# Performance work log

Measured on AMD Instinct MI355X. Metric: run time of the kernel, lower is better.

## Reference

```python
import jax, jax.numpy as jnp
import numpy as np

B, S, HID = 4, 8192, 1024
H, D = 16, 64
CHUNK = 64
N_BEFORE, N_AFTER = 1, 0
MASK_VALUE = -1e9


def look_adjacent(x, n_before, n_after):
    # x: [B, H, n_chunks, chunk, ...] -> concat rolled neighbor chunks along chunk-len dim
    if n_before == 0 and n_after == 0:
        return x
    slices = [jnp.roll(x, shift=-i, axis=2) for i in range(-n_before, n_after + 1)]
    return jnp.concatenate(slices, axis=3)


def setup_inputs() -> dict:
    key = jax.random.key(0)
    k0, k1, k2, k3 = jax.random.split(key, 4)
    scale = 1.0 / np.sqrt(HID)
    return {
        "hidden_states": jax.random.normal(k0, (B, S, HID), dtype=jnp.float32),
        "Wq": jax.random.normal(k1, (HID, HID), dtype=jnp.float32) * scale,
        "Wk": jax.random.normal(k2, (HID, HID), dtype=jnp.float32) * scale,
        "Wv": jax.random.normal(k3, (HID, HID), dtype=jnp.float32) * scale,
    }


def reference(hidden_states, Wq, Wk, Wv):
    b, s, _ = hidden_states.shape
    nC = s // CHUNK

    def split_heads(x):  # [B,S,HID] -> [B,H,S,D]
        return x.reshape(b, s, H, D).transpose(0, 2, 1, 3)

    q = split_heads(hidden_states @ Wq)
    k = split_heads(hidden_states @ Wk) / jnp.sqrt(jnp.asarray(D, hidden_states.dtype))
    v = split_heads(hidden_states @ Wv)

    # chunk: [B,H,nC,C,D]
    q = q.reshape(b, H, nC, CHUNK, D)
    k = k.reshape(b, H, nC, CHUNK, D)
    v = v.reshape(b, H, nC, CHUNK, D)

    idx = jnp.broadcast_to(jnp.arange(s), (b, H, s)).reshape(b, H, nC, CHUNK)
    q_idx = idx
    k_idx = look_adjacent(idx, N_BEFORE, N_AFTER)  # [B,H,nC,(1+nb+na)*C]
    k = look_adjacent(k, N_BEFORE, N_AFTER)        # [B,H,nC,(1+nb+na)*C,D]
    v = look_adjacent(v, N_BEFORE, N_AFTER)

    dots = jnp.einsum("bhncd,bhnkd->bhnck", q, k)  # [B,H,nC,C,K]
    causal = q_idx[..., :, None] >= k_idx[..., None, :]  # is_decoder causal mask
    dots = jnp.where(causal, dots, jnp.asarray(MASK_VALUE, dots.dtype))

    probs = jax.nn.softmax(dots, axis=-1)
    out = jnp.einsum("bhnck,bhnkd->bhncd", probs, v)  # [B,H,nC,C,D]
    out = out.reshape(b, H, s, D).transpose(0, 2, 1, 3).reshape(b, s, H * D)
    return out
```

## Files before the change

kernel.cpp:

```cpp
#include <hip/hip_runtime.h>
#include <hip/hip_bf16.h>

#define NB 4
#define NS 8192
#define NHID 1024
#define NH 16
#define ND 64
#define NCHUNK 128

typedef __attribute__((ext_vector_type(8))) __bf16 bf16x8;
typedef __attribute__((ext_vector_type(4))) float f32x4;

__device__ __forceinline__ unsigned short f2bf(float x) {
  unsigned int u = __builtin_bit_cast(unsigned int, x);
  unsigned int r = (u + 0x7FFFu + ((u >> 16) & 1u)) >> 16;
  return (unsigned short)r;
}

__device__ __forceinline__ void gload16(const void* g, void* l) {
  __builtin_amdgcn_global_load_lds(
      (const __attribute__((address_space(1))) unsigned int*)g,
      (__attribute__((address_space(3))) unsigned int*)l, 16, 0, 0);
}

#define BAR()                        \
  asm volatile("" ::: "memory");     \
  __builtin_amdgcn_s_barrier();      \
  asm volatile("" ::: "memory")

__global__ __launch_bounds__(256) void convert_x(const float* __restrict__ x,
                                                 unsigned short* __restrict__ xb) {
  int gt = blockIdx.x * 256 + threadIdx.x;
  const float4* xf = (const float4*)x;
  float4 v0 = xf[gt * 2 + 0];
  float4 v1 = xf[gt * 2 + 1];
  uint4 o;
  o.x = f2bf(v0.x) | ((unsigned)f2bf(v0.y) << 16);
  o.y = f2bf(v0.z) | ((unsigned)f2bf(v0.w) << 16);
  o.z = f2bf(v1.x) | ((unsigned)f2bf(v1.y) << 16);
  o.w = f2bf(v1.z) | ((unsigned)f2bf(v1.w) << 16);
  ((uint4*)xb)[gt] = o;
}

__global__ __launch_bounds__(256) void transpose_w(const float* __restrict__ w0,
                                                   const float* __restrict__ w1,
                                                   const float* __restrict__ w2,
                                                   unsigned short* __restrict__ wt) {
  __shared__ float tile[32][33];
  int wi = blockIdx.z;
  const float* w = (wi == 0) ? w0 : ((wi == 1) ? w1 : w2);
  float scale = (wi == 1) ? 0.125f : 1.0f;
  int k0 = blockIdx.x * 32, n0 = blockIdx.y * 32;
  int tx = threadIdx.x, ty = threadIdx.y;
#pragma unroll
  for (int i = 0; i < 4; i++)
    tile[ty + i * 8][tx] = w[(k0 + ty + i * 8) * NHID + n0 + tx];
  __syncthreads();
#pragma unroll
  for (int i = 0; i < 4; i++)
    wt[(wi * NHID + n0 + ty + i * 8) * NHID + k0 + tx] =
        f2bf(tile[tx][ty + i * 8] * scale);
}

#define OFF_A0 0
#define OFF_A1 16384
#define OFF_B0 32768
#define OFF_B1 49152

__device__ __forceinline__ void stage_half(const unsigned short* __restrict__ src,
                                           size_t row0, int kt, char* ldsbase,
                                           int tid) {
#pragma unroll
  for (int i = 0; i < 2; i++) {
    int g = tid + i * 512;
    int r = g >> 3;
    int slot = (g & 7) ^ (r & 7);
    gload16(src + (row0 + r) * NHID + kt * 64 + slot * 8, ldsbase + g * 16);
  }
}

__device__ __forceinline__ bf16x8 lds_frag(const char* base, int r, int ks,
                                           int lg) {
  int byte = (r * 128 + ks * 64 + lg * 16) ^ ((r & 7) << 4);
  return *reinterpret_cast<const bf16x8*>(base + byte);
}

#define MFMA16(ACC, AF, BF)                                                  \
  __builtin_amdgcn_s_setprio(1);                                            \
  _Pragma("unroll") for (int mi = 0; mi < 4; mi++)                          \
      _Pragma("unroll") for (int ni = 0; ni < 2; ni++)                      \
          _Pragma("unroll") for (int ks = 0; ks < 2; ks++)                  \
              ACC[mi][ni] = __builtin_amdgcn_mfma_f32_16x16x32_bf16(        \
                  AF[mi][ks], BF[ni][ks], ACC[mi][ni], 0, 0, 0);            \
  __builtin_amdgcn_s_setprio(0)

__global__ __launch_bounds__(512, 2) void gemm_qkv(
    const unsigned short* __restrict__ xb, const unsigned short* __restrict__ wt,
    unsigned short* __restrict__ qg, unsigned short* __restrict__ kg,
    unsigned short* __restrict__ vg) {
  __shared__ alignas(16) char smem[131072];
  int bid = blockIdx.x;
  int wg = (bid & 7) * 192 + (bid >> 3);
  int bm = wg / 12, bn = wg % 12;
  int tid = threadIdx.x;
  int l = tid & 63, lg = l >> 4, lm = l & 15;
  int w = tid >> 6, wm = w >> 2, wn = w & 3;

  const size_t arow0 = (size_t)bm * 256;
  const size_t brow0 = (size_t)bn * 256;

  stage_half(xb, arow0, 0, smem + OFF_A0, tid);
  stage_half(wt, brow0, 0, smem + OFF_B0, tid);
  stage_half(xb, arow0 + 128, 0, smem + OFF_A1, tid);
  stage_half(wt, brow0 + 128, 0, smem + OFF_B1, tid);
  stage_half(xb, arow0, 1, smem + 65536 + OFF_A0, tid);
  stage_half(wt, brow0, 1, smem + 65536 + OFF_B0, tid);
  asm volatile("s_waitcnt vmcnt(4)" ::: "memory");
  BAR();

  f32x4 acc[2][2][4][2] = {};
  bf16x8 a[4][2], b0[2][2], b1[2][2];

#pragma unroll 1
  for (int t = 0; t < 16; ++t) {
    char* cb = smem + (t & 1) * 65536;
    char* nb = smem + ((t & 1) ^ 1) * 65536;

#pragma unroll
    for (int mi = 0; mi < 4; mi++)
#pragma unroll
      for (int ks = 0; ks < 2; ks++)
        a[mi][ks] = lds_frag(cb + OFF_A0, wm * 64 + mi * 16 + lm, ks, lg);
#pragma unroll
    for (int ni = 0; ni < 2; ni++)
#pragma unroll
      for (int ks = 0; ks < 2; ks++)
        b0[ni][ks] = lds_frag(cb + OFF_B0, wn * 32 + ni * 16 + lm, ks, lg);
    if (t < 15) stage_half(xb, arow0 + 128, t + 1, nb + OFF_A1, tid);
    BAR();
    MFMA16(acc[0][0], a, b0);
    BAR();

#pragma unroll
    for (int ni = 0; ni < 2; ni++)
#pragma unroll
      for (int ks = 0; ks < 2; ks++)
        b1[ni][ks] = lds_frag(cb + OFF_B1, wn * 32 + ni * 16 + lm, ks, lg);
    if (t < 15) stage_half(wt, brow0 + 128, t + 1, nb + OFF_B1, tid);
    BAR();
    MFMA16(acc[0][1], a, b1);
    BAR();

#pragma unroll
    for (int mi = 0; mi < 4; mi++)
#pragma unroll
      for (int ks = 0; ks < 2; ks++)
        a[mi][ks] = lds_frag(cb + OFF_A1, wm * 64 + mi * 16 + lm, ks, lg);
    if (t < 14) stage_half(xb, arow0, t + 2, cb + OFF_A0, tid);
    BAR();
    MFMA16(acc[1][0], a, b0);
    BAR();

    if (t < 14) {
      stage_half(wt, brow0, t + 2, cb + OFF_B0, tid);
      asm volatile("s_waitcnt vmcnt(4)" ::: "memory");
    } else {
      asm volatile("s_waitcnt vmcnt(0)" ::: "memory");
    }
    BAR();
    MFMA16(acc[1][1], a, b1);
    BAR();
  }

  int wsel = bn >> 2;
  unsigned short* dst = (wsel == 0) ? qg : ((wsel == 1) ? kg : vg);
#pragma unroll
  for (int qm = 0; qm < 2; qm++)
#pragma unroll
    for (int qn = 0; qn < 2; qn++)
#pragma unroll
      for (int mi = 0; mi < 4; mi++)
#pragma unroll
        for (int ni = 0; ni < 2; ni++)
#pragma unroll
          for (int rr = 0; rr < 4; rr++) {
            int gm = bm * 256 + qm * 128 + wm * 64 + mi * 16 + lg * 4 + rr;
            int n = (bn & 3) * 256 + qn * 128 + wn * 32 + ni * 16 + lm;
            int b = gm >> 13, s = gm & (NS - 1);
            int h = n >> 6, d = n & (ND - 1);
            dst[(((size_t)(b * NH + h) * NS) + s) * ND + d] =
                f2bf(acc[qm][qn][mi][ni][rr]);
          }
}

__global__ __launch_bounds__(256, 4) void attn_local(
    const unsigned short* __restrict__ qg, const unsigned short* __restrict__ kg,
    const unsigned short* __restrict__ vg, float* __restrict__ out) {
  __shared__ alignas(16) char lds[40960];
  unsigned short* qs = (unsigned short*)lds;
  unsigned short* ks2 = (unsigned short*)(lds + 8192);
  unsigned short* vts = (unsigned short*)(lds + 24576);
  char* psb = lds;
  int c = blockIdx.x, h = blockIdx.y, b = blockIdx.z;
  int t = threadIdx.x;
  int w = t >> 6, l = t & 63, lg = l >> 4, lm = l & 15;
  size_t bhbase = (size_t)(b * NH + h) * NS * ND;
  int kv0 = (c - 1) * 64;

  int g0 = t, g1 = t + 256;
  int qrow0 = g0 >> 3, qcc0 = g0 & 7, qrow1 = g1 >> 3, qcc1 = g1 & 7;
  uint4 qv0 = *reinterpret_cast<const uint4*>(
      qg + bhbase + (size_t)(c * 64 + qrow0) * ND + qcc0 * 8);
  uint4 qv1 = *reinterpret_cast<const uint4*>(
      qg + bhbase + (size_t)(c * 64 + qrow1) * ND + qcc1 * 8);
  uint4 kvr[4];
  int krow[4], kcc[4];
#pragma unroll
  for (int i = 0; i < 4; i++) {
    int g = t + i * 256;
    krow[i] = g >> 3;
    kcc[i] = g & 7;
    int s = kv0 + krow[i];
    if (s < 0) s = 0;
    kvr[i] =
        *reinterpret_cast<const uint4*>(kg + bhbase + (size_t)s * ND + kcc[i] * 8);
  }
  int kq = t >> 1, half = t & 1;
  int sv = kv0 + kq;
  if (sv < 0) sv = 0;
  uint4 vreg[4];
#pragma unroll
  for (int i = 0; i < 4; i++)
    vreg[i] = *reinterpret_cast<const uint4*>(vg + bhbase + (size_t)sv * ND +
                                              half * 32 + i * 8);

  *reinterpret_cast<uint4*>(lds + ((qrow0 * 128 + qcc0 * 16) ^ ((qrow0 & 7) << 4))) =
      qv0;
  *reinterpret_cast<uint4*>(lds + ((qrow1 * 128 + qcc1 * 16) ^ ((qrow1 & 7) << 4))) =
      qv1;
#pragma unroll
  for (int i = 0; i < 4; i++)
    *reinterpret_cast<uint4*>(
        lds + 8192 + ((krow[i] * 128 + kcc[i] * 16) ^ ((krow[i] & 7) << 4))) =
        kvr[i];
  __syncthreads();

  bf16x8 qa[2];
#pragma unroll
  for (int ks = 0; ks < 2; ks++) {
    int row = w * 16 + lm;
    int byte = (row * 128 + (ks * 32 + lg * 8) * 2) ^ ((row & 7) << 4);
    qa[ks] = *reinterpret_cast<const bf16x8*>((char*)qs + byte);
  }
  f32x4 sf[8];
#pragma unroll
  for (int nt = 0; nt < 8; nt++) {
    f32x4 a = {};
#pragma unroll
    for (int ks = 0; ks < 2; ks++) {
      int n = nt * 16 + lm;
      int byte = (n * 128 + (ks * 32 + lg * 8) * 2) ^ ((n & 7) << 4);
      bf16x8 kb = *reinterpret_cast<const bf16x8*>((char*)ks2 + byte);
      a = __builtin_amdgcn_mfma_f32_16x16x32_bf16(kb, qa[ks], a, 0, 0, 0);
    }
    sf[nt] = a;
  }

  int q = w * 16 + lm;
  float m = -1e30f;
#pragma unroll
  for (int nt = 0; nt < 8; nt++)
#pragma unroll
    for (int r = 0; r < 4; r++) {
      int j = nt * 16 + lg * 4 + r;
      bool valid = (j <= q + 64) && (c > 0 || j >= 64);
      if (valid) m = fmaxf(m, sf[nt][r]);
    }
  m = fmaxf(m, __shfl_xor(m, 16, 64));
  m = fmaxf(m, __shfl_xor(m, 32, 64));

  float sum = 0.f;
#pragma unroll
  for (int nt = 0; nt < 8; nt++)
#pragma unroll
    for (int r = 0; r < 4; r++) {
      int j = nt * 16 + lg * 4 + r;
      bool valid = (j <= q + 64) && (c > 0 || j >= 64);
      float p = valid ? __expf(sf[nt][r] - m) : 0.0f;
      sf[nt][r] = p;
      sum += p;
    }
  sum += __shfl_xor(sum, 16, 64);
  sum += __shfl_xor(sum, 32, 64);
  float rn = 1.0f / sum;

  __syncthreads();

#pragma unroll
  for (int nt = 0; nt < 8; nt++) {
    unsigned int lo =
        f2bf(sf[nt][0] * rn) | ((unsigned)f2bf(sf[nt][1] * rn) << 16);
    unsigned int hi =
        f2bf(sf[nt][2] * rn) | ((unsigned)f2bf(sf[nt][3] * rn) << 16);
    int kvb = nt * 16 + lg * 4;
    int byte = (q * 256 + kvb * 2) ^ ((q & 7) << 4);
    *reinterpret_cast<uint2*>(psb + byte) = make_uint2(lo, hi);
  }
  {
    unsigned short* vtse = (unsigned short*)vts;
#pragma unroll
    for (int i = 0; i < 4; i++) {
      int d0 = half * 32 + i * 8;
      unsigned int u[4] = {vreg[i].x, vreg[i].y, vreg[i].z, vreg[i].w};
#pragma unroll
      for (int j = 0; j < 8; j++) {
        unsigned short val = (unsigned short)(u[j >> 1] >> ((j & 1) * 16));
        vtse[(d0 + j) * 128 + (kq ^ (j << 3))] = val;
      }
    }
  }
  __syncthreads();

  bf16x8 pa[4];
#pragma unroll
  for (int ks = 0; ks < 4; ks++) {
    int byte = (q * 256 + (ks * 32 + lg * 8) * 2) ^ ((q & 7) << 4);
    pa[ks] = *reinterpret_cast<const bf16x8*>(psb + byte);
  }
#pragma unroll
  for (int nt = 0; nt < 4; nt++) {
    f32x4 o = {};
#pragma unroll
    for (int ks = 0; ks < 4; ks++) {
      int dn = nt * 16 + lm;
      int byte = (dn * 256 + (ks * 32 + lg * 8) * 2) ^ ((dn & 7) << 4);
      bf16x8 vb = *reinterpret_cast<const bf16x8*>((char*)vts + byte);
      o = __builtin_amdgcn_mfma_f32_16x16x32_bf16(pa[ks], vb, o, 0, 0, 0);
    }
#pragma unroll
    for (int r = 0; r < 4; r++) {
      int sq = c * 64 + w * 16 + lg * 4 + r;
      int d = nt * 16 + lm;
      out[(size_t)(b * NS + sq) * (NH * ND) + h * ND + d] = o[r];
    }
  }
}

extern "C" void kernel_launch(void* const* d_in, const int* in_sizes, int n_in,
                              void* d_out, int out_size, void* d_ws, size_t ws_size,
                              hipStream_t stream) {
  const float* hs = (const float*)d_in[0];
  const float* wq = (const float*)d_in[1];
  const float* wk = (const float*)d_in[2];
  const float* wv = (const float*)d_in[3];
  float* out = (float*)d_out;
  char* ws = (char*)d_ws;

  const size_t XB_BYTES = (size_t)NB * NS * NHID * 2;
  const size_t WT_BYTES = (size_t)3 * NHID * NHID * 2;
  const size_t QKV_BYTES = (size_t)NB * NH * NS * ND * 2;
  unsigned short* xb = (unsigned short*)ws;
  unsigned short* wt = (unsigned short*)(ws + XB_BYTES);
  unsigned short* qg = (unsigned short*)(ws + XB_BYTES + WT_BYTES);
  unsigned short* kg = (unsigned short*)(ws + XB_BYTES + WT_BYTES + QKV_BYTES);
  unsigned short* vg = (unsigned short*)(ws + XB_BYTES + WT_BYTES + 2 * QKV_BYTES);

  hipLaunchKernelGGL(convert_x, dim3((NB * NS * NHID) / (256 * 8)), dim3(256), 0,
                     stream, hs, xb);
  hipLaunchKernelGGL(transpose_w, dim3(32, 32, 3), dim3(32, 8), 0, stream, wq, wk,
                     wv, wt);
  hipLaunchKernelGGL(gemm_qkv, dim3(128 * 12), dim3(512), 0, stream, xb, wt, qg,
                     kg, vg);
  hipLaunchKernelGGL(attn_local, dim3(NCHUNK, NH, NB), dim3(256), 0, stream, qg,
                     kg, vg, out);
}
```

Measured before the change: 498.5 us.

## Merge GEMM sub-phases to halve barriers and stage epilogue through LDS

The QKV projection GEMM main loop now issues both next-stage global-to-LDS loads up front and pairs the MFMA blocks, cutting the per-iteration barrier count from eight to four. The epilogue writes bf16 results into swizzled shared memory, then each thread stores 16-byte vectors to global instead of scattered 2-byte stores. This targets barrier stalls and uncoalesced output writes, at the cost of more live B fragments (register pressure) and an extra LDS round trip.

Result: no change. 505.3 us (+1.4%).

```diff
diff --git a/kernel.cpp b/kernel.cpp
--- a/kernel.cpp
+++ b/kernel.cpp
@@ -126,6 +126,10 @@
     char* cb = smem + (t & 1) * 65536;
     char* nb = smem + ((t & 1) ^ 1) * 65536;
 
+    if (t < 15) {
+      stage_half(xb, arow0 + 128, t + 1, nb + OFF_A1, tid);
+      stage_half(wt, brow0 + 128, t + 1, nb + OFF_B1, tid);
+    }
 #pragma unroll
     for (int mi = 0; mi < 4; mi++)
 #pragma unroll
@@ -134,63 +138,67 @@
 #pragma unroll
     for (int ni = 0; ni < 2; ni++)
 #pragma unroll
-      for (int ks = 0; ks < 2; ks++)
+      for (int ks = 0; ks < 2; ks++) {
         b0[ni][ks] = lds_frag(cb + OFF_B0, wn * 32 + ni * 16 + lm, ks, lg);
-    if (t < 15) stage_half(xb, arow0 + 128, t + 1, nb + OFF_A1, tid);
+        b1[ni][ks] = lds_frag(cb + OFF_B1, wn * 32 + ni * 16 + lm, ks, lg);
+      }
     BAR();
     MFMA16(acc[0][0], a, b0);
-    BAR();
-
-#pragma unroll
-    for (int ni = 0; ni < 2; ni++)
-#pragma unroll
-      for (int ks = 0; ks < 2; ks++)
-        b1[ni][ks] = lds_frag(cb + OFF_B1, wn * 32 + ni * 16 + lm, ks, lg);
-    if (t < 15) stage_half(wt, brow0 + 128, t + 1, nb + OFF_B1, tid);
-    BAR();
     MFMA16(acc[0][1], a, b1);
     BAR();
 
+    if (t < 14) {
+      stage_half(xb, arow0, t + 2, cb + OFF_A0, tid);
+      stage_half(wt, brow0, t + 2, cb + OFF_B0, tid);
+    }
 #pragma unroll
     for (int mi = 0; mi < 4; mi++)
 #pragma unroll
       for (int ks = 0; ks < 2; ks++)
         a[mi][ks] = lds_frag(cb + OFF_A1, wm * 64 + mi * 16 + lm, ks, lg);
-    if (t < 14) stage_half(xb, arow0, t + 2, cb + OFF_A0, tid);
-    BAR();
-    MFMA16(acc[1][0], a, b0);
-    BAR();
-
     if (t < 14) {
-      stage_half(wt, brow0, t + 2, cb + OFF_B0, tid);
       asm volatile("s_waitcnt vmcnt(4)" ::: "memory");
     } else {
       asm volatile("s_waitcnt vmcnt(0)" ::: "memory");
     }
     BAR();
+    MFMA16(acc[1][0], a, b0);
     MFMA16(acc[1][1], a, b1);
     BAR();
   }
 
+#pragma unroll
+  for (int qm = 0; qm < 2; qm++)
+#pragma unroll
+    for (int qn = 0; qn < 2; qn++)
+#pragma unroll
+      for (int mi = 0; mi < 4; mi++)
+#pragma unroll
+        for (int ni = 0; ni < 2; ni++)
+#pragma unroll
+          for (int rr = 0; rr < 4; rr++) {
+            int row = qm * 128 + wm * 64 + mi * 16 + lg * 4 + rr;
+            int col = qn * 128 + wn * 32 + ni * 16 + lm;
+            int byte = (row * 512 + col * 2) ^ ((row & 7) << 4);
+            *reinterpret_cast<unsigned short*>(smem + byte) =
+                f2bf(acc[qm][qn][mi][ni][rr]);
+          }
+  BAR();
   int wsel = bn >> 2;
   unsigned short* dst = (wsel == 0) ? qg : ((wsel == 1) ? kg : vg);
 #pragma unroll
-  for (int qm = 0; qm < 2; qm++)
-#pragma unroll
-    for (int qn = 0; qn < 2; qn++)
-#pragma unroll
-      for (int mi = 0; mi < 4; mi++)
-#pragma unroll
-        for (int ni = 0; ni < 2; ni++)
-#pragma unroll
-          for (int rr = 0; rr < 4; rr++) {
-            int gm = bm * 256 + qm * 128 + wm * 64 + mi * 16 + lg * 4 + rr;
-            int n = (bn & 3) * 256 + qn * 128 + wn * 32 + ni * 16 + lm;
-            int b = gm >> 13, s = gm & (NS - 1);
-            int h = n >> 6, d = n & (ND - 1);
-            dst[(((size_t)(b * NH + h) * NS) + s) * ND + d] =
-                f2bf(acc[qm][qn][mi][ni][rr]);
-          }
+  for (int it = 0; it < 16; ++it) {
+    int row = w * 32 + it * 2 + (l >> 5);
+    int colb = (l & 31) * 16;
+    int byte = (row * 512 + colb) ^ ((row & 7) << 4);
+    uint4 v = *reinterpret_cast<const uint4*>(smem + byte);
+    int gm = bm * 256 + row;
+    int b = gm >> 13, s = gm & (NS - 1);
+    int n = (bn & 3) * 256 + (colb >> 1);
+    int h = n >> 6, d = n & (ND - 1);
+    *reinterpret_cast<uint4*>(
+        &dst[(((size_t)(b * NH + h) * NS) + s) * ND + d]) = v;
+  }
 }
 
 __global__ __launch_bounds__(256, 4) void attn_local(
```
